# Performance work log

Hardware: AMD Instinct MI355X
Metric: run time of the kernel (lower is better)

## Reference

```python
import jax, jax.numpy as jnp
import numpy as np

TOKENS, D_MODEL, FC1, FC2 = 4096, 4096, 16384, 4096
EPS = 1e-3


def setup_inputs() -> dict:
    key = jax.random.key(0)
    ks = jax.random.split(key, 3)
    return {
        "inputs": jax.random.normal(ks[0], (TOKENS, D_MODEL), dtype=jnp.float32),
        "gamma": jnp.ones((D_MODEL,), dtype=jnp.float32),
        "beta": jnp.zeros((D_MODEL,), dtype=jnp.float32),
        "fc1_kernel": jax.random.normal(ks[1], (D_MODEL, FC1), dtype=jnp.float32) * 0.023,
        "fc1_bias": jnp.zeros((FC1,), dtype=jnp.float32),
        "fc2_kernel": jax.random.normal(ks[2], (FC1, FC2), dtype=jnp.float32) * 0.023,
        "fc2_bias": jnp.zeros((FC2,), dtype=jnp.float32),
    }


def _layernorm(x, gamma, beta):
    mu = jnp.mean(x, axis=-1, keepdims=True)
    var = jnp.mean(jnp.square(x - mu), axis=-1, keepdims=True)
    rsigma = jax.lax.rsqrt(var + EPS)
    return (x - mu) * rsigma * gamma + beta


def _gelu_tanh(x):
    # gelu with approximate=True (tanh approximation)
    c = jnp.asarray(0.7978845608028654, x.dtype)  # sqrt(2/pi)
    return 0.5 * x * (1.0 + jnp.tanh(c * (x + 0.044715 * x * x * x)))


def reference(inputs, gamma, beta, fc1_kernel, fc1_bias, fc2_kernel, fc2_bias):
    ln_out = _layernorm(inputs, gamma, beta)            # [T, D]
    fc1_out = jnp.matmul(ln_out, fc1_kernel) + fc1_bias  # [T, FC1]
    gelu_out = _gelu_tanh(fc1_out)
    fc2_out = jnp.matmul(gelu_out, fc2_kernel) + fc2_bias  # [T, FC2]
    return fc2_out
```

## Files before the change

### kernel.cpp

```cpp
#include <hip/hip_runtime.h>
#include <stdint.h>

#define TOKENS 4096
#define DMODEL 4096
#define FC1N   16384
#define FC2N   4096

typedef __attribute__((ext_vector_type(8))) __bf16 bf16x8;
typedef __attribute__((ext_vector_type(4))) float f32x4;

__device__ __forceinline__ unsigned short f2bf(float f) {
  unsigned u = __float_as_uint(f);
  u += 0x7fffu + ((u >> 16) & 1u);
  return (unsigned short)(u >> 16);
}

__device__ __forceinline__ float gelu_tanh(float x) {
  float y = 0.7978845608028654f * (x + 0.044715f * x * x * x);
  float e = __expf(2.0f * y);
  float t = 1.0f - 2.0f / (e + 1.0f);
  return 0.5f * x * (1.0f + t);
}

__global__ __launch_bounds__(256) void ln_kernel(const float* __restrict__ x,
                                                 const float* __restrict__ gamma,
                                                 const float* __restrict__ beta,
                                                 unsigned short* __restrict__ out) {
  const int row = blockIdx.x;
  const int tid = threadIdx.x;
  const float* xr = x + (size_t)row * DMODEL;
  float4 v[4];
  float s = 0.f, s2 = 0.f;
#pragma unroll
  for (int i = 0; i < 4; ++i) {
    v[i] = ((const float4*)xr)[tid + i * 256];
    s  += v[i].x + v[i].y + v[i].z + v[i].w;
    s2 += v[i].x * v[i].x + v[i].y * v[i].y + v[i].z * v[i].z + v[i].w * v[i].w;
  }
#pragma unroll
  for (int o = 32; o > 0; o >>= 1) {
    s  += __shfl_xor(s, o, 64);
    s2 += __shfl_xor(s2, o, 64);
  }
  __shared__ float red[2][4];
  const int wid = tid >> 6, lane = tid & 63;
  if (lane == 0) { red[0][wid] = s; red[1][wid] = s2; }
  __syncthreads();
  s  = red[0][0] + red[0][1] + red[0][2] + red[0][3];
  s2 = red[1][0] + red[1][1] + red[1][2] + red[1][3];
  const float mu = s * (1.f / DMODEL);
  const float var = s2 * (1.f / DMODEL) - mu * mu;
  const float rs = rsqrtf(var + 1e-3f);
  unsigned short* orow = out + (size_t)row * DMODEL;
#pragma unroll
  for (int i = 0; i < 4; ++i) {
    const int c4 = tid + i * 256;
    float4 g = ((const float4*)gamma)[c4];
    float4 b = ((const float4*)beta)[c4];
    ushort4 o;
    o.x = f2bf((v[i].x - mu) * rs * g.x + b.x);
    o.y = f2bf((v[i].y - mu) * rs * g.y + b.y);
    o.z = f2bf((v[i].z - mu) * rs * g.z + b.z);
    o.w = f2bf((v[i].w - mu) * rs * g.w + b.w);
    ((ushort4*)orow)[c4] = o;
  }
}

__global__ __launch_bounds__(256) void transpose_bf16(const float* __restrict__ W,
                                                      unsigned short* __restrict__ Wt,
                                                      int K, int N) {
  __shared__ float t[32][33];
  const int x = threadIdx.x & 31, y = threadIdx.x >> 5;
  const int n0 = blockIdx.x << 5, k0 = blockIdx.y << 5;
#pragma unroll
  for (int i = 0; i < 4; ++i)
    t[y + i * 8][x] = W[(size_t)(k0 + y + i * 8) * N + n0 + x];
  __syncthreads();
#pragma unroll
  for (int i = 0; i < 4; ++i)
    Wt[(size_t)(n0 + y + i * 8) * K + k0 + x] = f2bf(t[x][y + i * 8]);
}


__device__ __forceinline__ void stage_half(const unsigned short* __restrict__ src,
                                           int K, char* lds) {
  const int tid = threadIdx.x;
#pragma unroll
  for (int r = 0; r < 2; ++r) {
    const int o = ((r << 9) | tid) << 4;
    const int row = o >> 7;
    const int kb = (o & 127) ^ ((row & 7) << 4);
    const char* g = (const char*)(src + (size_t)row * K) + kb;
    __builtin_amdgcn_global_load_lds(
        (const __attribute__((address_space(1))) void*)g,
        (__attribute__((address_space(3))) void*)(lds + o), 16, 0, 0);
  }
}

__device__ __forceinline__ bf16x8 ldfrag(const char* tile, int row, int koff) {
  return *(const bf16x8*)(tile + row * 128 + (koff ^ ((row & 7) << 4)));
}

template <bool GELU>
__global__ __launch_bounds__(512, 2) void gemm256(const unsigned short* __restrict__ A,
                                                  const unsigned short* __restrict__ Bt,
                                                  const float* __restrict__ bias,
                                                  void* __restrict__ Cout,
                                                  int M, int N, int K) {
  extern __shared__ char smem[];
  const int tid = threadIdx.x;
  const int lane = tid & 63, wid = tid >> 6;
  const int lane15 = lane & 15, laneHi = lane >> 4;

  const int nwg = gridDim.x;
  const int bid = blockIdx.x;
  const int cpx = nwg >> 3;
  const int wg = (bid & 7) * cpx + (bid >> 3);
  const int nbx = N >> 8;
  const int bx = wg % nbx, by = wg / nbx;
  const int m0 = by << 8, n0 = bx << 8;
  const int wr = wid >> 2, wc = wid & 3;
  const int aRow0 = (wr << 7) + lane15;
  const int bRow0 = (wc << 6) + lane15;
  const int koffBase = laneHi << 4;

  const int NT = K >> 6;

  f32x4 acc[8][4];
#pragma unroll
  for (int m = 0; m < 8; ++m)
#pragma unroll
    for (int n = 0; n < 4; ++n) acc[m][n] = f32x4{0.f, 0.f, 0.f, 0.f};

  char* cur = smem;
  char* nxt = smem + 65536;

  stage_half(A  + (size_t)m0 * K,          K, cur);
  stage_half(Bt + (size_t)n0 * K,          K, cur + 32768);
  stage_half(A  + (size_t)(m0 + 128) * K,  K, cur + 16384);
  stage_half(Bt + (size_t)(n0 + 128) * K,  K, cur + 49152);
  stage_half(A  + (size_t)m0 * K + 64,     K, nxt);
  stage_half(Bt + (size_t)n0 * K + 64,     K, nxt + 32768);
  asm volatile("s_waitcnt vmcnt(4)" ::: "memory");
  __builtin_amdgcn_sched_barrier(0);
  __builtin_amdgcn_s_barrier();
  __builtin_amdgcn_sched_barrier(0);

  bf16x8 a[4][2], b0[2][2], b1[2][2];

  for (int t = 0; t < NT; ++t) {
    const char* Ab = cur;
    const char* Bb = cur + 32768;
    const int k1 = (t + 1) << 6, k2 = (t + 2) << 6;

#pragma unroll
    for (int m = 0; m < 4; ++m)
#pragma unroll
      for (int ks = 0; ks < 2; ++ks)
        a[m][ks] = ldfrag(Ab, aRow0 + m * 16, (ks << 6) | koffBase);
#pragma unroll
    for (int n = 0; n < 2; ++n)
#pragma unroll
      for (int ks = 0; ks < 2; ++ks)
        b0[n][ks] = ldfrag(Bb, bRow0 + n * 16, (ks << 6) | koffBase);
    if (t + 1 < NT) {
      stage_half(A  + (size_t)(m0 + 128) * K + k1, K, nxt + 16384);
      stage_half(Bt + (size_t)(n0 + 128) * K + k1, K, nxt + 49152);
    }
    __builtin_amdgcn_s_barrier();
    __builtin_amdgcn_s_setprio(1);
#pragma unroll
    for (int m = 0; m < 4; ++m)
#pragma unroll
      for (int n = 0; n < 2; ++n)
#pragma unroll
        for (int ks = 0; ks < 2; ++ks)
          acc[m][n] = __builtin_amdgcn_mfma_f32_16x16x32_bf16(a[m][ks], b0[n][ks], acc[m][n], 0, 0, 0);
    __builtin_amdgcn_s_setprio(0);
    __builtin_amdgcn_s_barrier();
    __builtin_amdgcn_sched_barrier(0);

#pragma unroll
    for (int n = 0; n < 2; ++n)
#pragma unroll
      for (int ks = 0; ks < 2; ++ks)
        b1[n][ks] = ldfrag(Bb, bRow0 + (n + 2) * 16, (ks << 6) | koffBase);
    __builtin_amdgcn_s_barrier();
    __builtin_amdgcn_s_setprio(1);
#pragma unroll
    for (int m = 0; m < 4; ++m)
#pragma unroll
      for (int n = 0; n < 2; ++n)
#pragma unroll
        for (int ks = 0; ks < 2; ++ks)
          acc[m][n + 2] = __builtin_amdgcn_mfma_f32_16x16x32_bf16(a[m][ks], b1[n][ks], acc[m][n + 2], 0, 0, 0);
    __builtin_amdgcn_s_setprio(0);
    __builtin_amdgcn_s_barrier();
    __builtin_amdgcn_sched_barrier(0);

#pragma unroll
    for (int m = 0; m < 4; ++m)
#pragma unroll
      for (int ks = 0; ks < 2; ++ks)
        a[m][ks] = ldfrag(Ab, aRow0 + (m + 4) * 16, (ks << 6) | koffBase);
    __builtin_amdgcn_s_barrier();
    __builtin_amdgcn_s_setprio(1);
#pragma unroll
    for (int m = 0; m < 4; ++m)
#pragma unroll
      for (int n = 0; n < 2; ++n)
#pragma unroll
        for (int ks = 0; ks < 2; ++ks)
          acc[m + 4][n + 2] = __builtin_amdgcn_mfma_f32_16x16x32_bf16(a[m][ks], b1[n][ks], acc[m + 4][n + 2], 0, 0, 0);
    __builtin_amdgcn_s_setprio(0);
    __builtin_amdgcn_s_barrier();
    __builtin_amdgcn_sched_barrier(0);

    if (t + 2 < NT) {
      stage_half(A  + (size_t)m0 * K + k2, K, cur);
      stage_half(Bt + (size_t)n0 * K + k2, K, cur + 32768);
      asm volatile("s_waitcnt vmcnt(4)" ::: "memory");
    } else {
      asm volatile("s_waitcnt vmcnt(0)" ::: "memory");
    }
    __builtin_amdgcn_sched_barrier(0);
    __builtin_amdgcn_s_barrier();
    __builtin_amdgcn_s_setprio(1);
#pragma unroll
    for (int m = 0; m < 4; ++m)
#pragma unroll
      for (int n = 0; n < 2; ++n)
#pragma unroll
        for (int ks = 0; ks < 2; ++ks)
          acc[m + 4][n] = __builtin_amdgcn_mfma_f32_16x16x32_bf16(a[m][ks], b0[n][ks], acc[m + 4][n], 0, 0, 0);
    __builtin_amdgcn_s_setprio(0);
    __builtin_amdgcn_s_barrier();
    __builtin_amdgcn_sched_barrier(0);

    char* tmp = cur; cur = nxt; nxt = tmp;
  }

#pragma unroll
  for (int nf = 0; nf < 4; ++nf) {
    const int col = n0 + (wc << 6) + (nf << 4) + lane15;
    const float bs = bias[col];
#pragma unroll
    for (int mf = 0; mf < 8; ++mf) {
      const int rbase = m0 + (wr << 7) + (mf << 4) + (laneHi << 2);
#pragma unroll
      for (int j = 0; j < 4; ++j) {
        const float v = acc[mf][nf][j] + bs;
        if (GELU) {
          ((unsigned short*)Cout)[(size_t)(rbase + j) * N + col] = f2bf(gelu_tanh(v));
        } else {
          ((float*)Cout)[(size_t)(rbase + j) * N + col] = v;
        }
      }
    }
  }
}

extern "C" void kernel_launch(void* const* d_in, const int* in_sizes, int n_in,
                              void* d_out, int out_size, void* d_ws, size_t ws_size,
                              hipStream_t stream) {
  const float* x     = (const float*)d_in[0];
  const float* gamma = (const float*)d_in[1];
  const float* beta  = (const float*)d_in[2];
  const float* w1    = (const float*)d_in[3];
  const float* b1    = (const float*)d_in[4];
  const float* w2    = (const float*)d_in[5];
  const float* b2    = (const float*)d_in[6];

  unsigned short* lnout = (unsigned short*)d_ws;
  unsigned short* gout  = (unsigned short*)((char*)d_ws + (size_t)32  * 1024 * 1024);
  unsigned short* wT    = (unsigned short*)((char*)d_ws + (size_t)160 * 1024 * 1024);

  (void)hipFuncSetAttribute((const void*)gemm256<true>,
                            hipFuncAttributeMaxDynamicSharedMemorySize, 131072);
  (void)hipFuncSetAttribute((const void*)gemm256<false>,
                            hipFuncAttributeMaxDynamicSharedMemorySize, 131072);

  ln_kernel<<<TOKENS, 256, 0, stream>>>(x, gamma, beta, lnout);

  transpose_bf16<<<dim3(FC1N / 32, DMODEL / 32), 256, 0, stream>>>(w1, wT, DMODEL, FC1N);
  gemm256<true><<<dim3((TOKENS / 256) * (FC1N / 256)), 512, 131072, stream>>>(
      lnout, wT, b1, (void*)gout, TOKENS, FC1N, DMODEL);

  transpose_bf16<<<dim3(FC2N / 32, FC1N / 32), 256, 0, stream>>>(w2, wT, FC1N, FC2N);
  gemm256<false><<<dim3((TOKENS / 256) * (FC2N / 256)), 512, 131072, stream>>>(
      gout, wT, b2, d_out, TOKENS, FC2N, FC1N);
}
```

Baseline: 1.207 ms.

## Restructure GEMM main loop to preload all fragments and prefetch next tile A

```diff
diff --git a/kernel.cpp b/kernel.cpp
--- a/kernel.cpp
+++ b/kernel.cpp
@@ -135,104 +135,111 @@
   char* cur = smem;
   char* nxt = smem + 65536;
 
-  stage_half(A  + (size_t)m0 * K,          K, cur);
-  stage_half(Bt + (size_t)n0 * K,          K, cur + 32768);
-  stage_half(A  + (size_t)(m0 + 128) * K,  K, cur + 16384);
-  stage_half(Bt + (size_t)(n0 + 128) * K,  K, cur + 49152);
-  stage_half(A  + (size_t)m0 * K + 64,     K, nxt);
-  stage_half(Bt + (size_t)n0 * K + 64,     K, nxt + 32768);
-  asm volatile("s_waitcnt vmcnt(4)" ::: "memory");
+  stage_half(A  + (size_t)m0 * K,               K, cur);
+  stage_half(A  + (size_t)(m0 + 128) * K,       K, cur + 16384);
+  stage_half(Bt + (size_t)n0 * K,               K, cur + 32768);
+  stage_half(Bt + (size_t)(n0 + 128) * K,       K, cur + 49152);
+  stage_half(A  + (size_t)m0 * K + 64,          K, nxt);
+  stage_half(A  + (size_t)(m0 + 128) * K + 64,  K, nxt + 16384);
+  stage_half(Bt + (size_t)n0 * K + 64,          K, nxt + 32768);
+  stage_half(Bt + (size_t)(n0 + 128) * K + 64,  K, nxt + 49152);
+  asm volatile("s_waitcnt vmcnt(8)" ::: "memory");
   __builtin_amdgcn_sched_barrier(0);
   __builtin_amdgcn_s_barrier();
   __builtin_amdgcn_sched_barrier(0);
 
-  bf16x8 a[4][2], b0[2][2], b1[2][2];
+  bf16x8 alo[4][2], ahi[4][2], blo[2][2], bhi[2][2];
+
+#pragma unroll
+  for (int m = 0; m < 4; ++m)
+#pragma unroll
+    for (int ks = 0; ks < 2; ++ks)
+      alo[m][ks] = ldfrag(cur, aRow0 + m * 16, (ks << 6) | koffBase);
 
   for (int t = 0; t < NT; ++t) {
-    const char* Ab = cur;
     const char* Bb = cur + 32768;
-    const int k1 = (t + 1) << 6, k2 = (t + 2) << 6;
-
-#pragma unroll
-    for (int m = 0; m < 4; ++m)
+    const int k2 = (t + 2) << 6;
+
+#pragma unroll
+    for (int n = 0; n < 2; ++n)
 #pragma unroll
       for (int ks = 0; ks < 2; ++ks)
-        a[m][ks] = ldfrag(Ab, aRow0 + m * 16, (ks << 6) | koffBase);
+        blo[n][ks] = ldfrag(Bb, bRow0 + n * 16, (ks << 6) | koffBase);
 #pragma unroll
     for (int n = 0; n < 2; ++n)
 #pragma unroll
       for (int ks = 0; ks < 2; ++ks)
-        b0[n][ks] = ldfrag(Bb, bRow0 + n * 16, (ks << 6) | koffBase);
-    if (t + 1 < NT) {
-      stage_half(A  + (size_t)(m0 + 128) * K + k1, K, nxt + 16384);
-      stage_half(Bt + (size_t)(n0 + 128) * K + k1, K, nxt + 49152);
-    }
-    __builtin_amdgcn_s_barrier();
-    __builtin_amdgcn_s_setprio(1);
-#pragma unroll
-    for (int m = 0; m < 4; ++m)
-#pragma unroll
-      for (int n = 0; n < 2; ++n)
-#pragma unroll
-        for (int ks = 0; ks < 2; ++ks)
-          acc[m][n] = __builtin_amdgcn_mfma_f32_16x16x32_bf16(a[m][ks], b0[n][ks], acc[m][n], 0, 0, 0);
-    __builtin_amdgcn_s_setprio(0);
-    __builtin_amdgcn_s_barrier();
-    __builtin_amdgcn_sched_barrier(0);
-
-#pragma unroll
-    for (int n = 0; n < 2; ++n)
+        bhi[n][ks] = ldfrag(Bb, bRow0 + (n + 2) * 16, (ks << 6) | koffBase);
+#pragma unroll
+    for (int m = 0; m < 4; ++m)
 #pragma unroll
       for (int ks = 0; ks < 2; ++ks)
-        b1[n][ks] = ldfrag(Bb, bRow0 + (n + 2) * 16, (ks << 6) | koffBase);
-    __builtin_amdgcn_s_barrier();
-    __builtin_amdgcn_s_setprio(1);
-#pragma unroll
-    for (int m = 0; m < 4; ++m)
-#pragma unroll
-      for (int n = 0; n < 2; ++n)
-#pragma unroll
-        for (int ks = 0; ks < 2; ++ks)
-          acc[m][n + 2] = __builtin_amdgcn_mfma_f32_16x16x32_bf16(a[m][ks], b1[n][ks], acc[m][n + 2], 0, 0, 0);
-    __builtin_amdgcn_s_setprio(0);
-    __builtin_amdgcn_s_barrier();
-    __builtin_amdgcn_sched_barrier(0);
-
-#pragma unroll
-    for (int m = 0; m < 4; ++m)
-#pragma unroll
-      for (int ks = 0; ks < 2; ++ks)
-        a[m][ks] = ldfrag(Ab, aRow0 + (m + 4) * 16, (ks << 6) | koffBase);
-    __builtin_amdgcn_s_barrier();
-    __builtin_amdgcn_s_setprio(1);
-#pragma unroll
-    for (int m = 0; m < 4; ++m)
-#pragma unroll
-      for (int n = 0; n < 2; ++n)
-#pragma unroll
-        for (int ks = 0; ks < 2; ++ks)
-          acc[m + 4][n + 2] = __builtin_amdgcn_mfma_f32_16x16x32_bf16(a[m][ks], b1[n][ks], acc[m + 4][n + 2], 0, 0, 0);
-    __builtin_amdgcn_s_setprio(0);
-    __builtin_amdgcn_s_barrier();
-    __builtin_amdgcn_sched_barrier(0);
+        ahi[m][ks] = ldfrag(cur, aRow0 + (m + 4) * 16, (ks << 6) | koffBase);
+    __builtin_amdgcn_s_barrier();
+    __builtin_amdgcn_s_setprio(1);
+#pragma unroll
+    for (int m = 0; m < 4; ++m)
+#pragma unroll
+      for (int n = 0; n < 2; ++n)
+#pragma unroll
+        for (int ks = 0; ks < 2; ++ks)
+          acc[m][n] = __builtin_amdgcn_mfma_f32_16x16x32_bf16(alo[m][ks], blo[n][ks], acc[m][n], 0, 0, 0);
+    __builtin_amdgcn_s_setprio(0);
+    __builtin_amdgcn_s_barrier();
+
+    __builtin_amdgcn_s_setprio(1);
+#pragma unroll
+    for (int m = 0; m < 4; ++m)
+#pragma unroll
+      for (int n = 0; n < 2; ++n)
+#pragma unroll
+        for (int ks = 0; ks < 2; ++ks)
+          acc[m][n + 2] = __builtin_amdgcn_mfma_f32_16x16x32_bf16(alo[m][ks], bhi[n][ks], acc[m][n + 2], 0, 0, 0);
+    __builtin_amdgcn_s_setprio(0);
+    __builtin_amdgcn_s_barrier();
 
     if (t + 2 < NT) {
       stage_half(A  + (size_t)m0 * K + k2, K, cur);
       stage_half(Bt + (size_t)n0 * K + k2, K, cur + 32768);
+    }
+    __builtin_amdgcn_s_barrier();
+    __builtin_amdgcn_s_setprio(1);
+#pragma unroll
+    for (int m = 0; m < 4; ++m)
+#pragma unroll
+      for (int n = 0; n < 2; ++n)
+#pragma unroll
+        for (int ks = 0; ks < 2; ++ks)
+          acc[m + 4][n + 2] = __builtin_amdgcn_mfma_f32_16x16x32_bf16(ahi[m][ks], bhi[n][ks], acc[m + 4][n + 2], 0, 0, 0);
+    __builtin_amdgcn_s_setprio(0);
+    if (t + 2 < NT) {
       asm volatile("s_waitcnt vmcnt(4)" ::: "memory");
-    } else {
+    } else if (t + 1 < NT) {
       asm volatile("s_waitcnt vmcnt(0)" ::: "memory");
     }
     __builtin_amdgcn_sched_barrier(0);
     __builtin_amdgcn_s_barrier();
-    __builtin_amdgcn_s_setprio(1);
-#pragma unroll
-    for (int m = 0; m < 4; ++m)
-#pragma unroll
-      for (int n = 0; n < 2; ++n)
-#pragma unroll
-        for (int ks = 0; ks < 2; ++ks)
-          acc[m + 4][n] = __builtin_amdgcn_mfma_f32_16x16x32_bf16(a[m][ks], b0[n][ks], acc[m + 4][n], 0, 0, 0);
+    __builtin_amdgcn_sched_barrier(0);
+
+    if (t + 1 < NT) {
+#pragma unroll
+      for (int m = 0; m < 4; ++m)
+#pragma unroll
+        for (int ks = 0; ks < 2; ++ks)
+          alo[m][ks] = ldfrag(nxt, aRow0 + m * 16, (ks << 6) | koffBase);
+    }
+    if (t + 2 < NT) {
+      stage_half(A  + (size_t)(m0 + 128) * K + k2, K, cur + 16384);
+      stage_half(Bt + (size_t)(n0 + 128) * K + k2, K, cur + 49152);
+    }
+    __builtin_amdgcn_s_setprio(1);
+#pragma unroll
+    for (int m = 0; m < 4; ++m)
+#pragma unroll
+      for (int n = 0; n < 2; ++n)
+#pragma unroll
+        for (int ks = 0; ks < 2; ++ks)
+          acc[m + 4][n] = __builtin_amdgcn_mfma_f32_16x16x32_bf16(ahi[m][ks], blo[n][ks], acc[m + 4][n], 0, 0, 0);
     __builtin_amdgcn_s_setprio(0);
     __builtin_amdgcn_s_barrier();
     __builtin_amdgcn_sched_barrier(0);
```

New measurement: 1.221 ms. Within noise of the previous version (+1.2%).
